# Performance work log

Hardware: AMD Instinct MI355X
Metric: run time of the kernel (lower is better)

The kernel has to match this reference:

```python
import jax, jax.numpy as jnp
import numpy as np


def setup_inputs() -> dict:
    key = jax.random.key(0)
    k1, k2, k3 = jax.random.split(key, 3)
    N = 20000
    # valid [x1, y1, x2, y2] boxes: centers in [0,1000), sizes in [1,101)
    xy = jax.random.uniform(k1, (N, 2), dtype=jnp.float32) * 1000.0
    wh = jax.random.uniform(k2, (N, 2), dtype=jnp.float32) * 100.0 + 1.0
    boxes = jnp.concatenate([xy, xy + wh], axis=1)
    scores = jax.random.uniform(k3, (N,), dtype=jnp.float32)
    return {
        "boxes": boxes,
        "scores": scores,
        "max_output_size": 1000,
        "iou_threshold": 0.5,
        "scores_threshold": 0.1,
    }


def reference(boxes, scores, max_output_size, iou_threshold, scores_threshold):
    boxes = boxes.astype(jnp.float32)
    scores = scores.astype(jnp.float32)
    N = boxes.shape[0]

    # score filtering: instead of physically filtering (dynamic shape),
    # mark below-threshold boxes as pre-suppressed and push them to the
    # end of the stable descending sort with -inf keys.
    valid = scores > scores_threshold
    sort_key = jnp.where(valid, scores, -jnp.inf)
    order = jnp.argsort(-sort_key)  # jnp.argsort is stable -> stable descending

    sboxes = boxes[order]                      # [N,4] score-sorted boxes
    svalid = valid[order]
    sorig = order.astype(jnp.int32)            # original indices, sorted
    areas = (sboxes[:, 2] - sboxes[:, 0]) * (sboxes[:, 3] - sboxes[:, 1])
    idx = jnp.arange(N)

    def body(carry, i):
        suppressed, selected, count = carry
        can = jnp.logical_and(~suppressed[i], count < max_output_size)
        selected = jnp.where(can, selected.at[count].set(sorig[i]), selected)
        # vectorized IoU of box i against all boxes (only j > i matter)
        b = sboxes[i]
        x1 = jnp.maximum(b[0], sboxes[:, 0])
        y1 = jnp.maximum(b[1], sboxes[:, 1])
        x2 = jnp.minimum(b[2], sboxes[:, 2])
        y2 = jnp.minimum(b[3], sboxes[:, 3])
        inter = jnp.maximum(x2 - x1, 0.0) * jnp.maximum(y2 - y1, 0.0)
        union = jnp.maximum(areas[i] + areas - inter, 1e-6)
        iou = inter / union
        suppressed = suppressed | (can & (idx > i) & (iou >= iou_threshold))
        count = count + can.astype(jnp.int32)
        return (suppressed, selected, count), None

    init = (~svalid, jnp.zeros(max_output_size, dtype=jnp.int32), jnp.int32(0))
    (_, selected, count), _ = jax.lax.scan(body, init, idx)
    return selected, count
```

## Files before the change

kernel.cpp:

```cpp
#include <hip/hip_runtime.h>
#include <cstdint>

typedef unsigned long long u64;

#define TOPK 2048
#define MW2 (TOPK / 64)
#define CAND 4096
#define HIST_BLOCKS 8
#define COMPACT_BLOCKS 32
#define RANK_BLOCKS (CAND / 64)
#define NTILES ((MW2 * (MW2 + 1)) / 2)
#define FB_WORDS 1024
#define SCAN_NT 256


__device__ __forceinline__ unsigned score_ud(float s, float thr) {
    unsigned u = __float_as_uint(s);
    u ^= (u >> 31) ? 0xFFFFFFFFu : 0x80000000u;
    unsigned ud = ~u;
    if (!(s > thr)) ud = 0xFFFFFFFFu;
    return ud;
}

__global__ __launch_bounds__(256) void hist_kernel(const float* __restrict__ scores,
                                                   const float* __restrict__ thrPtr,
                                                   int* __restrict__ slices,
                                                   int* __restrict__ meta, int N) {
    __shared__ int h[4096];
    int tid = threadIdx.x;
    for (int b = tid; b < 4096; b += 256) h[b] = 0;
    if (blockIdx.x == 0 && tid == 0) meta[0] = 0;
    __syncthreads();
    float thr = *thrPtr;
    for (int i = blockIdx.x * 256 + tid; i < N; i += HIST_BLOCKS * 256) {
        unsigned ud = score_ud(scores[i], thr);
        if (ud != 0xFFFFFFFFu) atomicAdd(&h[ud >> 20], 1);
    }
    __syncthreads();
    int* myslice = slices + blockIdx.x * 4096;
    for (int b = tid; b < 4096; b += 256) myslice[b] = h[b];
}

__global__ __launch_bounds__(256) void compact_kernel(
        const float* __restrict__ scores, const float* __restrict__ thrPtr,
        const int* __restrict__ slices, int* __restrict__ meta,
        u64* __restrict__ ckeys, int N, int maxNeed) {
    __shared__ int bins[4096];
    __shared__ int shC;
    int tid = threadIdx.x, lane = tid & 63;
    {
        const int4* sl = (const int4*)slices;
        int4* bo = (int4*)bins;
#pragma unroll
        for (int k = 0; k < 4; ++k) {
            int p = k * 256 + tid;
            int4 a = sl[p];
            int4 v1 = sl[1024 + p];
            int4 v2 = sl[2 * 1024 + p];
            int4 v3 = sl[3 * 1024 + p];
            int4 v4 = sl[4 * 1024 + p];
            int4 v5 = sl[5 * 1024 + p];
            int4 v6 = sl[6 * 1024 + p];
            int4 v7 = sl[7 * 1024 + p];
            a.x += v1.x + v2.x + v3.x + v4.x + v5.x + v6.x + v7.x;
            a.y += v1.y + v2.y + v3.y + v4.y + v5.y + v6.y + v7.y;
            a.z += v1.z + v2.z + v3.z + v4.z + v5.z + v6.z + v7.z;
            a.w += v1.w + v2.w + v3.w + v4.w + v5.w + v6.w + v7.w;
            bo[p] = a;
        }
    }
    __syncthreads();
    if (tid < 64) {
        int base = lane * 64;
        int sum = 0;
        for (int b = 0; b < 64; ++b) sum += bins[base + ((b + lane) & 63)];
        int incl = sum;
        for (int off = 1; off < 64; off <<= 1) {
            int o = __shfl_up(incl, off, 64);
            if (lane >= off) incl += o;
        }
        int total = __shfl(incl, 63, 64);
        int need = (maxNeed < total) ? maxNeed : total;
        u64 ok = __ballot(incl >= need);
        int L = (ok != 0ull) ? (int)__builtin_ctzll(ok) : 0;
        if (lane == L) {
            int acc = incl - sum;
            int C = base, Msel = acc;
            for (int b = 0; b < 64; ++b) {
                acc += bins[base + b];
                if (acc >= need) { C = base + b; Msel = acc; break; }
            }
            if (need <= 0) { C = -1; Msel = 0; }
            shC = C;
            if (blockIdx.x == 0) {
                meta[2] = Msel;
                meta[3] = (Msel > CAND) ? 1 : 0;
            }
        }
        if (lane == 0 && blockIdx.x == 0) meta[1] = total;
    }
    __syncthreads();
    int C = shC;
    float thr = *thrPtr;
    for (int i0 = blockIdx.x * 256; i0 < N; i0 += COMPACT_BLOCKS * 256) {
        int i = i0 + tid;
        bool sel = false;
        unsigned ud = 0;
        if (i < N) {
            ud = score_ud(scores[i], thr);
            sel = (ud != 0xFFFFFFFFu) && ((int)(ud >> 20) <= C);
        }
        u64 ball = __ballot(sel);
        if (ball) {
            int cntw = __popcll(ball);
            int base = 0;
            if (lane == 0) base = atomicAdd(&meta[0], cntw);
            base = __shfl(base, 0, 64);
            if (sel) {
                int slot = base + __popcll(ball & ((1ull << lane) - 1ull));
                if (slot < CAND) ckeys[slot] = ((u64)ud << 32) | (unsigned)i;
            }
        }
    }
}

__global__ __launch_bounds__(256) void rank_gather_kernel(
        const u64* __restrict__ ckeys, const int* __restrict__ meta,
        const float* __restrict__ boxes,
        float4* __restrict__ sboxes, int* __restrict__ sorig) {
    __shared__ u64 lk[CAND];
    __shared__ int part[4][64];
    int tid = threadIdx.x, lane = tid & 63, q = tid >> 6;
    int Msel = meta[2];
    if (Msel > CAND) Msel = CAND;
    for (int j = tid; j < Msel; j += 256) lk[j] = ckeys[j];
    __syncthreads();
    if (blockIdx.x * 64 >= Msel) return;
    int i = blockIdx.x * 64 + lane;
    u64 key = (i < Msel) ? lk[i] : ~0ull;
    int chunk = (Msel + 3) >> 2;
    int j0 = q * chunk;
    int j1 = j0 + chunk; if (j1 > Msel) j1 = Msel;
    int r = 0;
#pragma unroll 4
    for (int j = j0; j < j1; ++j) r += (lk[j] < key) ? 1 : 0;
    part[q][lane] = r;
    __syncthreads();
    if (q == 0 && i < Msel) {
        int rank = part[0][lane] + part[1][lane] + part[2][lane] + part[3][lane];
        if (rank < TOPK) {
            int idx = (int)(key & 0xFFFFFFFFu);
            sboxes[rank] = ((const float4*)boxes)[idx];
            sorig[rank] = idx;
        }
    }
}

__global__ __launch_bounds__(64) void mask2_kernel(
        const float4* __restrict__ sboxes, const float* __restrict__ iouThrPtr,
        u64* __restrict__ maskT, u64* __restrict__ diagT) {
    __shared__ float jx1[64], jy1[64], jx2[64], jy2[64], ja[64];
    __shared__ u64 rowLDS[64];
    int t = threadIdx.x;
    int wi = 0, tt = blockIdx.x;
    while (tt >= MW2 - wi) { tt -= MW2 - wi; ++wi; }
    int wj = wi + tt;
    int j0 = wj << 6;
    float4 jb = sboxes[j0 + t];
    jx1[t] = jb.x; jy1[t] = jb.y; jx2[t] = jb.z; jy2[t] = jb.w;
    ja[t] = (jb.z - jb.x) * (jb.w - jb.y);
    __syncthreads();
    int i = (wi << 6) + t;
    float thr = *iouThrPtr;
    float4 ib = sboxes[i];
    float ia = (ib.z - ib.x) * (ib.w - ib.y);
    u64 bits = 0;
    for (int jj = 0; jj < 64; ++jj) {
        int j = j0 + jj;
        if (j > i) {
            float xx1 = fmaxf(ib.x, jx1[jj]);
            float yy1 = fmaxf(ib.y, jy1[jj]);
            float xx2 = fminf(ib.z, jx2[jj]);
            float yy2 = fminf(ib.w, jy2[jj]);
            float ww = fmaxf(xx2 - xx1, 0.0f);
            float hh = fmaxf(yy2 - yy1, 0.0f);
            float inter = ww * hh;
            float uni = fmaxf(ia + ja[jj] - inter, 1e-6f);
            if (inter / uni >= thr) bits |= 1ull << jj;
        }
    }
    rowLDS[t] = bits;
    __syncthreads();
    u64 col = 0;
    for (int r = 0; r < 64; ++r) col |= ((rowLDS[r] >> t) & 1ull) << r;
    maskT[(size_t)(j0 + t) * MW2 + wi] = col;
    if (wi == wj) diagT[(wi << 6) + t] = col;
}

__global__ __launch_bounds__(SCAN_NT) void scan2_kernel(
        const u64* __restrict__ maskT, const u64* __restrict__ diagT,
        const int* __restrict__ sorig, const int* __restrict__ meta,
        const float* __restrict__ boxes, const float* __restrict__ scores,
        const float* __restrict__ iouThrPtr, const float* __restrict__ scoreThrPtr,
        int* __restrict__ out, int N, int maxOut) {
    __shared__ u64 diagLDS[TOPK];
    __shared__ u64 selw[MW2];
    __shared__ u64 validwLDS[MW2];
    __shared__ u64 ballots[4];
    __shared__ int selLDS[TOPK];
    __shared__ int cntSh;
    __shared__ u64 aliveW[FB_WORDS];
    __shared__ u64 keyRed[4];
    __shared__ u64 winKeySh;
    int tid = threadIdx.x, lane = tid & 63, wave = tid >> 6;

    int Msel = meta[2];
    int V = (Msel < TOPK) ? Msel : TOPK;
    for (int k = tid; k < TOPK; k += SCAN_NT) diagLDS[k] = diagT[k];
    if (tid < MW2) {
        int lo = tid * 64;
        u64 vw = (V >= lo + 64) ? ~0ull : ((V > lo) ? ((1ull << (V - lo)) - 1ull) : 0ull);
        validwLDS[tid] = vw;
        selw[tid] = 0ull;
    }
    if (tid == 0) cntSh = 0;

    ulonglong2 a0, a1, a2, a3;
    int cc = tid >> 2, g = tid & 3;
    {
        const ulonglong2* p = (const ulonglong2*)(maskT + (size_t)cc * MW2 + g * 8);
        a0 = p[0]; a1 = p[1]; a2 = p[2]; a3 = p[3];
    }
    __syncthreads();

    int cnt = 0;
    for (int w = 0; w < MW2; ++w) {
        {
            u64 wd0 = a0.x, wd1 = a0.y, wd2 = a1.x, wd3 = a1.y;
            u64 wd4 = a2.x, wd5 = a2.y, wd6 = a3.x, wd7 = a3.y;
            int wr0 = g * 8;
            u64 acc = 0;
            if (wr0 + 0 < w) acc |= wd0 & selw[wr0 + 0];
            if (wr0 + 1 < w) acc |= wd1 & selw[wr0 + 1];
            if (wr0 + 2 < w) acc |= wd2 & selw[wr0 + 2];
            if (wr0 + 3 < w) acc |= wd3 & selw[wr0 + 3];
            if (wr0 + 4 < w) acc |= wd4 & selw[wr0 + 4];
            if (wr0 + 5 < w) acc |= wd5 & selw[wr0 + 5];
            if (wr0 + 6 < w) acc |= wd6 & selw[wr0 + 6];
            if (wr0 + 7 < w) acc |= wd7 & selw[wr0 + 7];
            acc |= __shfl_xor(acc, 1, 64);
            acc |= __shfl_xor(acc, 2, 64);
            u64 B = __ballot(acc != 0ull);
            if (lane == 0) ballots[wave] = B;
            if (w + 1 < MW2) {
                const ulonglong2* p = (const ulonglong2*)(maskT + (size_t)((w + 1) * 64 + cc) * MW2 + g * 8);
                a0 = p[0]; a1 = p[1]; a2 = p[2]; a3 = p[3];
            }
        }
        __syncthreads();
        if (wave == 0) {
            u64 bv = ballots[lane >> 4];
            bool crossk = (bv >> ((lane & 15) << 2)) & 1ull;
            bool alv = ((validwLDS[w] >> lane) & 1ull) && !crossk;
            u64 inm = diagLDS[(w << 6) | lane];
            u64 sel = __ballot(alv);
            for (int it = 0; it < 64; ++it) {
                bool killed = (inm & sel) != 0ull;
                u64 ns = __ballot(alv && !killed);
                if (ns == sel) break;
                sel = ns;
            }
            int room = maxOut - cnt;
            int tot = __popcll(sel);
            u64 below = (1ull << lane) - 1ull;
            if (tot > room) {
                bool keep = ((sel >> lane) & 1ull) && (__popcll(sel & below) < room);
                sel = __ballot(keep);
                tot = room;
            }
            if ((sel >> lane) & 1ull) {
                int pos = cnt + __popcll(sel & below);
                selLDS[pos] = (w << 6) | lane;
            }
            if (lane == 0) { selw[w] = sel; cntSh = cnt + tot; }
        }
        __syncthreads();
        cnt = cntSh;
        if (cnt >= maxOut) break;
    }

    int vt = meta[1];
    int f2 = meta[3];
    bool complete = (f2 == 0) && ((cnt >= maxOut) || (V >= vt));
    if (complete) {
        for (int k = tid; k < cnt; k += SCAN_NT) out[k] = sorig[selLDS[k]];
        for (int k = cnt + tid; k < maxOut; k += SCAN_NT) out[k] = 0;
        if (tid == 0) out[maxOut] = cnt;
        return;
    }

    float sThr = *scoreThrPtr, iThr = *iouThrPtr;
    for (int e0 = wave << 6; e0 < N; e0 += SCAN_NT) {
        int e = e0 + lane;
        bool a = (e < N) && (scores[e] > sThr);
        u64 ball = __ballot(a);
        if (lane == 0) aliveW[e0 >> 6] = ball;
    }
    __syncthreads();
    int fcnt = 0;
    while (fcnt < maxOut) {
        u64 best = 0;
        for (int e = tid; e < N; e += SCAN_NT) {
            if ((aliveW[e >> 6] >> (e & 63)) & 1ull) {
                float s = scores[e];
                unsigned u = __float_as_uint(s);
                u ^= (u >> 31) ? 0xFFFFFFFFu : 0x80000000u;
                u64 k = ((u64)u << 32) | (unsigned)(~e);
                if (k > best) best = k;
            }
        }
#pragma unroll
        for (int off = 32; off >= 1; off >>= 1) {
            u64 o = __shfl_xor(best, off, 64);
            if (o > best) best = o;
        }
        if (lane == 0) keyRed[wave] = best;
        __syncthreads();
        if (tid == 0) {
            u64 b = 0;
            for (int p = 0; p < 4; ++p) if (keyRed[p] > b) b = keyRed[p];
            winKeySh = b;
        }
        __syncthreads();
        u64 wk = winKeySh;
        if (wk == 0ull) break;
        int win = (int)(~(unsigned)wk);
        if (tid == 0) out[fcnt] = win;
        ++fcnt;
        float4 wb = ((const float4*)boxes)[win];
        float wa = (wb.z - wb.x) * (wb.w - wb.y);
        for (int e0 = wave << 6; e0 < N; e0 += SCAN_NT) {
            int e = e0 + lane;
            bool kill = false;
            if (e < N && ((aliveW[e0 >> 6] >> lane) & 1ull)) {
                if (e == win) kill = true;
                else {
                    float4 bb = ((const float4*)boxes)[e];
                    float xx1 = fmaxf(wb.x, bb.x), yy1 = fmaxf(wb.y, bb.y);
                    float xx2 = fminf(wb.z, bb.z), yy2 = fminf(wb.w, bb.w);
                    float inter = fmaxf(xx2 - xx1, 0.0f) * fmaxf(yy2 - yy1, 0.0f);
                    float ba = (bb.z - bb.x) * (bb.w - bb.y);
                    float uni = fmaxf(wa + ba - inter, 1e-6f);
                    kill = (inter / uni >= iThr);
                }
            }
            u64 kb = __ballot(kill);
            if (lane == 0 && kb) aliveW[e0 >> 6] &= ~kb;
        }
        __syncthreads();
    }
    for (int k = fcnt + tid; k < maxOut; k += SCAN_NT) out[k] = 0;
    if (tid == 0) out[maxOut] = fcnt;
}

extern "C" void kernel_launch(void* const* d_in, const int* in_sizes, int n_in,
                              void* d_out, int out_size, void* d_ws, size_t ws_size,
                              hipStream_t stream) {
    const float* boxes       = (const float*)d_in[0];
    const float* scores      = (const float*)d_in[1];
    const float* iouThrPtr   = (const float*)d_in[3];
    const float* scoreThrPtr = (const float*)d_in[4];

    int N = in_sizes[0] / 4;
    int maxOut = out_size - 1;

    char* ws = (char*)d_ws;
    size_t off = 0;
    auto take = [&](size_t b) { void* p = ws + off; off = (off + b + 255) & ~(size_t)255; return p; };
    int*    slices = (int*)   take((size_t)HIST_BLOCKS * 4096 * 4);
    int*    meta   = (int*)   take(256);
    u64*    ckeys  = (u64*)   take((size_t)CAND * 8);
    float4* sboxes = (float4*)take((size_t)TOPK * 16);
    int*    sorig  = (int*)   take((size_t)TOPK * 4);
    u64*    maskT  = (u64*)   take((size_t)TOPK * MW2 * 8);
    u64*    diagT  = (u64*)   take((size_t)MW2 * 64 * 8);
    (void)ws_size;

    hist_kernel<<<HIST_BLOCKS, 256, 0, stream>>>(scores, scoreThrPtr, slices, meta, N);
    compact_kernel<<<COMPACT_BLOCKS, 256, 0, stream>>>(scores, scoreThrPtr, slices, meta,
                                                       ckeys, N, TOPK);
    rank_gather_kernel<<<RANK_BLOCKS, 256, 0, stream>>>(ckeys, meta, boxes, sboxes, sorig);
    mask2_kernel<<<NTILES, 64, 0, stream>>>(sboxes, iouThrPtr, maskT, diagT);
    scan2_kernel<<<1, SCAN_NT, 0, stream>>>(maskT, diagT, sorig, meta,
                                            boxes, scores, iouThrPtr, scoreThrPtr,
                                            (int*)d_out, N, maxOut);
}
```

Measured before the change: 64.67 us.

## Replace histogram threshold pass with sampled cutoff and per-segment compaction

Result: slower. 83.58 us (+29.2%).

```diff
diff --git a/kernel.cpp b/kernel.cpp
--- a/kernel.cpp
+++ b/kernel.cpp
@@ -5,10 +5,11 @@
 
 #define TOPK 2048
 #define MW2 (TOPK / 64)
-#define CAND 4096
-#define HIST_BLOCKS 8
-#define COMPACT_BLOCKS 32
-#define RANK_BLOCKS (CAND / 64)
+#define CAND 8192
+#define NSEG 32
+#define SEGSZ (CAND / NSEG)
+#define SAMPLE 512
+#define RANKB (CAND / 64)
 #define NTILES ((MW2 * (MW2 + 1)) / 2)
 #define FB_WORDS 1024
 #define SCAN_NT 256
@@ -22,131 +23,119 @@
     return ud;
 }
 
-__global__ __launch_bounds__(256) void hist_kernel(const float* __restrict__ scores,
-                                                   const float* __restrict__ thrPtr,
-                                                   int* __restrict__ slices,
-                                                   int* __restrict__ meta, int N) {
-    __shared__ int h[4096];
-    int tid = threadIdx.x;
-    for (int b = tid; b < 4096; b += 256) h[b] = 0;
-    if (blockIdx.x == 0 && tid == 0) meta[0] = 0;
-    __syncthreads();
-    float thr = *thrPtr;
-    for (int i = blockIdx.x * 256 + tid; i < N; i += HIST_BLOCKS * 256) {
-        unsigned ud = score_ud(scores[i], thr);
-        if (ud != 0xFFFFFFFFu) atomicAdd(&h[ud >> 20], 1);
-    }
-    __syncthreads();
-    int* myslice = slices + blockIdx.x * 4096;
-    for (int b = tid; b < 4096; b += 256) myslice[b] = h[b];
-}
-
 __global__ __launch_bounds__(256) void compact_kernel(
         const float* __restrict__ scores, const float* __restrict__ thrPtr,
-        const int* __restrict__ slices, int* __restrict__ meta,
-        u64* __restrict__ ckeys, int N, int maxNeed) {
-    __shared__ int bins[4096];
-    __shared__ int shC;
-    int tid = threadIdx.x, lane = tid & 63;
-    {
-        const int4* sl = (const int4*)slices;
-        int4* bo = (int4*)bins;
-#pragma unroll
-        for (int k = 0; k < 4; ++k) {
-            int p = k * 256 + tid;
-            int4 a = sl[p];
-            int4 v1 = sl[1024 + p];
-            int4 v2 = sl[2 * 1024 + p];
-            int4 v3 = sl[3 * 1024 + p];
-            int4 v4 = sl[4 * 1024 + p];
-            int4 v5 = sl[5 * 1024 + p];
-            int4 v6 = sl[6 * 1024 + p];
-            int4 v7 = sl[7 * 1024 + p];
-            a.x += v1.x + v2.x + v3.x + v4.x + v5.x + v6.x + v7.x;
-            a.y += v1.y + v2.y + v3.y + v4.y + v5.y + v6.y + v7.y;
-            a.z += v1.z + v2.z + v3.z + v4.z + v5.z + v6.z + v7.z;
-            a.w += v1.w + v2.w + v3.w + v4.w + v5.w + v6.w + v7.w;
-            bo[p] = a;
-        }
-    }
-    __syncthreads();
+        int* __restrict__ meta, u64* __restrict__ ckeys, int N) {
+    __shared__ u64 skeys[SAMPLE];
+    __shared__ int shC, validSamp, ticket, validC;
+    int tid = threadIdx.x, lane = tid & 63, bid = blockIdx.x;
+    float thr = *thrPtr;
+    if (tid == 0) { shC = 0xFFE; validSamp = 0; ticket = 0; validC = 0; }
+    __syncthreads();
+    for (int k = tid; k < SAMPLE; k += 256) {
+        int idx = (int)(((long long)k * N) / SAMPLE);
+        unsigned ud = score_ud(scores[idx], thr);
+        skeys[k] = ((u64)ud << 32) | (unsigned)idx;
+    }
+    __syncthreads();
+    int tr = (int)((3048LL * SAMPLE + N - 1) / N);
+    if (tr < 1) tr = 1; if (tr > SAMPLE) tr = SAMPLE;
+    int myv = 0;
+    for (int k = tid; k < SAMPLE; k += 256) {
+        u64 key = skeys[k];
+        bool valid = ((unsigned)(key >> 32) != 0xFFFFFFFFu);
+        if (valid) ++myv;
+        int r = 0;
+#pragma unroll 8
+        for (int j = 0; j < SAMPLE; ++j) r += (skeys[j] < key) ? 1 : 0;
+        if (valid && r == tr - 1) shC = (int)(key >> 52);
+    }
+    if (myv) atomicAdd(&validSamp, myv);
+    __syncthreads();
+    int sv = validSamp;
+    int C = (N <= CAND || ((long long)sv * N) / SAMPLE < 6500) ? 0xFFE : shC;
+    int lo = (int)(((long long)N * bid) / NSEG);
+    int hi = (int)(((long long)N * (bid + 1)) / NSEG);
+    for (int i0 = lo; i0 < hi; i0 += 256) {
+        int i = i0 + tid;
+        bool inb = (i < hi);
+        unsigned ud = 0;
+        bool valid = false, sel = false;
+        if (inb) {
+            ud = score_ud(scores[i], thr);
+            valid = (ud != 0xFFFFFFFFu);
+            sel = valid && ((int)(ud >> 20) <= C);
+        }
+        u64 vb = __ballot(valid);
+        u64 sb = __ballot(sel);
+        if (lane == 0 && vb) atomicAdd(&validC, __popcll(vb));
+        if (sb) {
+            int base = 0;
+            if (lane == 0) base = atomicAdd(&ticket, __popcll(sb));
+            base = __shfl(base, 0, 64);
+            if (sel) {
+                int slot = base + __popcll(sb & ((1ull << lane) - 1ull));
+                if (slot < SEGSZ) ckeys[bid * SEGSZ + slot] = ((u64)ud << 32) | (unsigned)i;
+            }
+        }
+    }
+    __syncthreads();
+    if (tid == 0) {
+        int t = ticket;
+        meta[8 + bid]  = (t < SEGSZ) ? t : SEGSZ;
+        meta[40 + bid] = validC;
+        meta[72 + bid] = (t > SEGSZ) ? 1 : 0;
+    }
+}
+
+__global__ __launch_bounds__(256) void rank_gather_kernel(
+        const u64* __restrict__ ckeys, int* __restrict__ meta,
+        const float* __restrict__ boxes,
+        float4* __restrict__ sboxes, int* __restrict__ sorig) {
+    __shared__ u64 lk[CAND];
+    __shared__ int segOff[NSEG + 1];
+    __shared__ int part[4][64];
+    __shared__ int shVT, shF2;
+    int tid = threadIdx.x, lane = tid & 63, wave = tid >> 6, bid = blockIdx.x;
     if (tid < 64) {
-        int base = lane * 64;
-        int sum = 0;
-        for (int b = 0; b < 64; ++b) sum += bins[base + ((b + lane) & 63)];
-        int incl = sum;
+        int c = (lane < NSEG) ? meta[8 + lane]  : 0;
+        int f = (lane < NSEG) ? meta[72 + lane] : 0;
+        int v = (lane < NSEG) ? meta[40 + lane] : 0;
+        int incl = c;
         for (int off = 1; off < 64; off <<= 1) {
             int o = __shfl_up(incl, off, 64);
             if (lane >= off) incl += o;
         }
-        int total = __shfl(incl, 63, 64);
-        int need = (maxNeed < total) ? maxNeed : total;
-        u64 ok = __ballot(incl >= need);
-        int L = (ok != 0ull) ? (int)__builtin_ctzll(ok) : 0;
-        if (lane == L) {
-            int acc = incl - sum;
-            int C = base, Msel = acc;
-            for (int b = 0; b < 64; ++b) {
-                acc += bins[base + b];
-                if (acc >= need) { C = base + b; Msel = acc; break; }
-            }
-            if (need <= 0) { C = -1; Msel = 0; }
-            shC = C;
-            if (blockIdx.x == 0) {
-                meta[2] = Msel;
-                meta[3] = (Msel > CAND) ? 1 : 0;
-            }
-        }
-        if (lane == 0 && blockIdx.x == 0) meta[1] = total;
-    }
-    __syncthreads();
-    int C = shC;
-    float thr = *thrPtr;
-    for (int i0 = blockIdx.x * 256; i0 < N; i0 += COMPACT_BLOCKS * 256) {
-        int i = i0 + tid;
-        bool sel = false;
-        unsigned ud = 0;
-        if (i < N) {
-            ud = score_ud(scores[i], thr);
-            sel = (ud != 0xFFFFFFFFu) && ((int)(ud >> 20) <= C);
-        }
-        u64 ball = __ballot(sel);
-        if (ball) {
-            int cntw = __popcll(ball);
-            int base = 0;
-            if (lane == 0) base = atomicAdd(&meta[0], cntw);
-            base = __shfl(base, 0, 64);
-            if (sel) {
-                int slot = base + __popcll(ball & ((1ull << lane) - 1ull));
-                if (slot < CAND) ckeys[slot] = ((u64)ud << 32) | (unsigned)i;
-            }
-        }
-    }
-}
-
-__global__ __launch_bounds__(256) void rank_gather_kernel(
-        const u64* __restrict__ ckeys, const int* __restrict__ meta,
-        const float* __restrict__ boxes,
-        float4* __restrict__ sboxes, int* __restrict__ sorig) {
-    __shared__ u64 lk[CAND];
-    __shared__ int part[4][64];
-    int tid = threadIdx.x, lane = tid & 63, q = tid >> 6;
-    int Msel = meta[2];
-    if (Msel > CAND) Msel = CAND;
-    for (int j = tid; j < Msel; j += 256) lk[j] = ckeys[j];
-    __syncthreads();
-    if (blockIdx.x * 64 >= Msel) return;
-    int i = blockIdx.x * 64 + lane;
+        if (lane < NSEG) segOff[lane] = incl - c;
+        if (lane == NSEG - 1) segOff[NSEG] = incl;
+#pragma unroll
+        for (int off = 32; off >= 1; off >>= 1) {
+            f |= __shfl_xor(f, off, 64);
+            v += __shfl_xor(v, off, 64);
+        }
+        if (lane == 0) { shF2 = f; shVT = v; }
+    }
+    __syncthreads();
+    int Msel = segOff[NSEG];
+    if (bid == 0 && tid == 0) { meta[1] = shVT; meta[2] = Msel; meta[3] = shF2; }
+    if (bid * 64 >= Msel) return;
+    for (int s = 0; s < NSEG; ++s) {
+        int base = segOff[s];
+        int cnt = segOff[s + 1] - base;
+        for (int j = tid; j < cnt; j += 256) lk[base + j] = ckeys[s * SEGSZ + j];
+    }
+    __syncthreads();
+    int i = bid * 64 + lane;
     u64 key = (i < Msel) ? lk[i] : ~0ull;
     int chunk = (Msel + 3) >> 2;
-    int j0 = q * chunk;
+    int j0 = wave * chunk;
     int j1 = j0 + chunk; if (j1 > Msel) j1 = Msel;
     int r = 0;
 #pragma unroll 4
     for (int j = j0; j < j1; ++j) r += (lk[j] < key) ? 1 : 0;
-    part[q][lane] = r;
-    __syncthreads();
-    if (q == 0 && i < Msel) {
+    part[wave][lane] = r;
+    __syncthreads();
+    if (wave == 0 && i < Msel) {
         int rank = part[0][lane] + part[1][lane] + part[2][lane] + part[3][lane];
         if (rank < TOPK) {
             int idx = (int)(key & 0xFFFFFFFFu);
@@ -377,8 +366,7 @@
     char* ws = (char*)d_ws;
     size_t off = 0;
     auto take = [&](size_t b) { void* p = ws + off; off = (off + b + 255) & ~(size_t)255; return p; };
-    int*    slices = (int*)   take((size_t)HIST_BLOCKS * 4096 * 4);
-    int*    meta   = (int*)   take(256);
+    int*    meta   = (int*)   take(1024);
     u64*    ckeys  = (u64*)   take((size_t)CAND * 8);
     float4* sboxes = (float4*)take((size_t)TOPK * 16);
     int*    sorig  = (int*)   take((size_t)TOPK * 4);
@@ -386,10 +374,8 @@
     u64*    diagT  = (u64*)   take((size_t)MW2 * 64 * 8);
     (void)ws_size;
 
-    hist_kernel<<<HIST_BLOCKS, 256, 0, stream>>>(scores, scoreThrPtr, slices, meta, N);
-    compact_kernel<<<COMPACT_BLOCKS, 256, 0, stream>>>(scores, scoreThrPtr, slices, meta,
-                                                       ckeys, N, TOPK);
-    rank_gather_kernel<<<RANK_BLOCKS, 256, 0, stream>>>(ckeys, meta, boxes, sboxes, sorig);
+    compact_kernel<<<NSEG, 256, 0, stream>>>(scores, scoreThrPtr, meta, ckeys, N);
+    rank_gather_kernel<<<RANKB, 256, 0, stream>>>(ckeys, meta, boxes, sboxes, sorig);
     mask2_kernel<<<NTILES, 64, 0, stream>>>(sboxes, iouThrPtr, maskT, diagT);
     scan2_kernel<<<1, SCAN_NT, 0, stream>>>(maskT, diagT, sorig, meta,
                                             boxes, scores, iouThrPtr, scoreThrPtr,
```
